# Optimization experiments

Measured on AMD Instinct MI355X. Metric: run time of the kernel, lower is better.

Reference implementation:

```python
import jax, jax.numpy as jnp
import numpy as np

N_NODES = 100000
N_EDGES = 1600000
IN_CH = 128
HEADS = 4
HID = 32
OUT_CH = 128
NEG_SLOPE = 0.2


def setup_inputs() -> dict:
    key = jax.random.key(0)
    ks = jax.random.split(key, 7)
    sc = 1.0 / np.sqrt(IN_CH)
    return {
        "x": jax.random.normal(ks[0], (N_NODES, IN_CH), dtype=jnp.float32),
        "edge_index": jax.random.randint(ks[1], (2, N_EDGES), 0, N_NODES, dtype=jnp.int32),
        "W": jax.random.normal(ks[2], (IN_CH, HEADS * HID), dtype=jnp.float32) * sc,
        "att_src": jax.random.normal(ks[3], (HEADS, HID), dtype=jnp.float32) * sc,
        "att_dst": jax.random.normal(ks[4], (HEADS, HID), dtype=jnp.float32) * sc,
        "lin_w": jax.random.normal(ks[5], (HEADS * HID, OUT_CH), dtype=jnp.float32) * (1.0 / np.sqrt(HEADS * HID)),
        "lin_b": jax.random.normal(ks[6], (OUT_CH,), dtype=jnp.float32) * 0.01,
    }


def reference(x, edge_index, W, att_src, att_dst, lin_w, lin_b):
    N = x.shape[0]
    src, dst = edge_index[0], edge_index[1]
    # node-wise linear transform -> [N, H, C]
    h = (x @ W).reshape(N, HEADS, HID)
    # per-node attention logit components [N, H]
    a_src = jnp.einsum("nhc,hc->nh", h, att_src)
    a_dst = jnp.einsum("nhc,hc->nh", h, att_dst)
    # per-edge logits with LeakyReLU [E, H]
    e = jax.nn.leaky_relu(a_src[src] + a_dst[dst], negative_slope=NEG_SLOPE)
    # segment softmax over destination neighborhoods
    m = jax.ops.segment_max(e, dst, num_segments=N)
    ex = jnp.exp(e - m[dst])
    s = jax.ops.segment_sum(ex, dst, num_segments=N)
    alpha = ex / (s[dst] + 1e-16)
    # weighted scatter-sum of source features [N, H, C] -> concat heads
    msg = h[src] * alpha[:, :, None]
    out = jax.ops.segment_sum(msg, dst, num_segments=N).reshape(N, HEADS * HID)
    # trailing dense + ReLU
    return jax.nn.relu(out @ lin_w + lin_b)
```

## Files before the change

kernel.cpp:

```cpp
#include <hip/hip_runtime.h>
#include <hip/hip_fp16.h>

#define NB   256
#define NBLK 128
#define BSH  9

typedef _Float16 f16;
typedef _Float16 half8 __attribute__((ext_vector_type(8)));
typedef __fp16 pk16x2 __attribute__((ext_vector_type(2)));
typedef float f32x4 __attribute__((ext_vector_type(4)));

__global__ void k_prep(const float* __restrict__ W, const float* __restrict__ LW,
                       f16* __restrict__ Wt, f16* __restrict__ LWt)
{
    int n = blockIdx.x & 127;
    const float* src = (blockIdx.x < 128) ? W : LW;
    f16* dst = (blockIdx.x < 128) ? Wt : LWt;
    int k = threadIdx.x;
    dst[n * 128 + k] = (f16)src[k * 128 + n];
}

__global__ __launch_bounds__(256) void k_gemm_att(
    const float* __restrict__ A, const f16* __restrict__ Wt,
    const float* __restrict__ att_s, const float* __restrict__ att_d,
    f16* __restrict__ Hh, float* __restrict__ as_out, float* __restrict__ ad_out,
    int M)
{
    __shared__ __align__(16) f16 as_lds[64 * 136];
    int t = threadIdx.x;
    int row0 = blockIdx.x * 64;

    {
        int r = t >> 2, kq = (t & 3) * 32;
        const float* ap = A + (size_t)(row0 + r) * 128 + kq;
        bool valid = (row0 + r) < M;
        pk16x2 hb[16];
#pragma unroll
        for (int j = 0; j < 8; ++j) {
            float4 v = valid ? *(const float4*)(ap + j * 4) : make_float4(0.f, 0.f, 0.f, 0.f);
            hb[2 * j]     = __builtin_amdgcn_cvt_pkrtz(v.x, v.y);
            hb[2 * j + 1] = __builtin_amdgcn_cvt_pkrtz(v.z, v.w);
        }
        f16* dst = as_lds + r * 136 + kq;
#pragma unroll
        for (int j = 0; j < 4; ++j) *(float4*)(dst + j * 8) = ((float4*)hb)[j];
    }
    __syncthreads();

    int w = t >> 6, ln = t & 63;
    int rr = (w & 1) * 32;
    int cc = (w >> 1) * 64;
    int q = ln >> 4, m = ln & 15;

    f32x4 acc[2][4];
#pragma unroll
    for (int i = 0; i < 2; ++i)
#pragma unroll
        for (int j = 0; j < 4; ++j) acc[i][j] = (f32x4){0.f, 0.f, 0.f, 0.f};

    const f16* wp = Wt + (size_t)(cc + m) * 128 + q * 8;
#pragma unroll
    for (int ks = 0; ks < 4; ++ks) {
        int k0 = ks * 32 + q * 8;
        half8 a0 = *(const half8*)(as_lds + (rr + m) * 136 + k0);
        half8 a1 = *(const half8*)(as_lds + (rr + 16 + m) * 136 + k0);
        half8 bf[4];
#pragma unroll
        for (int j = 0; j < 4; ++j)
            bf[j] = *(const half8*)(wp + j * 16 * 128 + ks * 32);
#pragma unroll
        for (int j = 0; j < 4; ++j) {
            acc[0][j] = __builtin_amdgcn_mfma_f32_16x16x32_f16(a0, bf[j], acc[0][j], 0, 0, 0);
            acc[1][j] = __builtin_amdgcn_mfma_f32_16x16x32_f16(a1, bf[j], acc[1][j], 0, 0, 0);
        }
    }
    __syncthreads();
#pragma unroll
    for (int i = 0; i < 2; ++i)
#pragma unroll
        for (int j = 0; j < 4; ++j)
#pragma unroll
            for (int g = 0; g < 4; ++g)
                as_lds[(rr + i * 16 + q * 4 + g) * 136 + cc + j * 16 + m] = (f16)acc[i][j][g];
    __syncthreads();
    {
        int r = t >> 2, cq = (t & 3) * 32;
        if (row0 + r < M) {
            float4 o0 = *(const float4*)(as_lds + r * 136 + cq);
            float4 o1 = *(const float4*)(as_lds + r * 136 + cq + 8);
            float4 o2 = *(const float4*)(as_lds + r * 136 + cq + 16);
            float4 o3 = *(const float4*)(as_lds + r * 136 + cq + 24);
            float4* hp = (float4*)(Hh + (size_t)(row0 + r) * 128 + cq);
            hp[0] = o0; hp[1] = o1; hp[2] = o2; hp[3] = o3;
        }
    }
    {
        int rl = w * 16 + m;
        int head = q;
        float ds = 0.f, dd = 0.f;
#pragma unroll
        for (int ch = 0; ch < 4; ++ch) {
            half8 hv = *(const half8*)(as_lds + rl * 136 + head * 32 + ch * 8);
            float4 s0 = *(const float4*)(att_s + head * 32 + ch * 8);
            float4 s1 = *(const float4*)(att_s + head * 32 + ch * 8 + 4);
            float4 d0 = *(const float4*)(att_d + head * 32 + ch * 8);
            float4 d1 = *(const float4*)(att_d + head * 32 + ch * 8 + 4);
            ds += (float)hv[0] * s0.x + (float)hv[1] * s0.y + (float)hv[2] * s0.z + (float)hv[3] * s0.w
                + (float)hv[4] * s1.x + (float)hv[5] * s1.y + (float)hv[6] * s1.z + (float)hv[7] * s1.w;
            dd += (float)hv[0] * d0.x + (float)hv[1] * d0.y + (float)hv[2] * d0.z + (float)hv[3] * d0.w
                + (float)hv[4] * d1.x + (float)hv[5] * d1.y + (float)hv[6] * d1.z + (float)hv[7] * d1.w;
        }
        if (row0 + rl < M) {
            as_out[(row0 + rl) * 4 + head] = ds;
            ad_out[(row0 + rl) * 4 + head] = dd;
        }
    }
}

__global__ __launch_bounds__(256) void k_gemm_bias_relu(
    const f16* __restrict__ Ah, const f16* __restrict__ LWt,
    const float* __restrict__ bias, float* __restrict__ Out, int M)
{
    __shared__ __align__(16) f16 as_lds[64 * 136];
    int t = threadIdx.x;
    int row0 = blockIdx.x * 64;
    {
        int r = t >> 2, kq = (t & 3) * 32;
        f16* dst = as_lds + r * 136 + kq;
        if (row0 + r < M) {
            const float4* ap = (const float4*)(Ah + (size_t)(row0 + r) * 128 + kq);
#pragma unroll
            for (int j = 0; j < 4; ++j) *(float4*)(dst + j * 8) = ap[j];
        } else {
            float4 z = make_float4(0.f, 0.f, 0.f, 0.f);
#pragma unroll
            for (int j = 0; j < 4; ++j) *(float4*)(dst + j * 8) = z;
        }
    }
    __syncthreads();

    int w = t >> 6, ln = t & 63;
    int rr = (w & 1) * 32;
    int cc = (w >> 1) * 64;
    int q = ln >> 4, m = ln & 15;

    f32x4 acc[2][4];
#pragma unroll
    for (int i = 0; i < 2; ++i)
#pragma unroll
        for (int j = 0; j < 4; ++j) acc[i][j] = (f32x4){0.f, 0.f, 0.f, 0.f};

    const f16* wp = LWt + (size_t)(cc + m) * 128 + q * 8;
#pragma unroll
    for (int ks = 0; ks < 4; ++ks) {
        int k0 = ks * 32 + q * 8;
        half8 a0 = *(const half8*)(as_lds + (rr + m) * 136 + k0);
        half8 a1 = *(const half8*)(as_lds + (rr + 16 + m) * 136 + k0);
        half8 bf[4];
#pragma unroll
        for (int j = 0; j < 4; ++j)
            bf[j] = *(const half8*)(wp + j * 16 * 128 + ks * 32);
#pragma unroll
        for (int j = 0; j < 4; ++j) {
            acc[0][j] = __builtin_amdgcn_mfma_f32_16x16x32_f16(a0, bf[j], acc[0][j], 0, 0, 0);
            acc[1][j] = __builtin_amdgcn_mfma_f32_16x16x32_f16(a1, bf[j], acc[1][j], 0, 0, 0);
        }
    }
    float bv[4];
#pragma unroll
    for (int j = 0; j < 4; ++j) bv[j] = bias[cc + j * 16 + m];
#pragma unroll
    for (int i = 0; i < 2; ++i)
#pragma unroll
        for (int g = 0; g < 4; ++g) {
            int row = row0 + rr + i * 16 + q * 4 + g;
            if (row < M) {
#pragma unroll
                for (int j = 0; j < 4; ++j)
                    Out[(size_t)row * 128 + cc + j * 16 + m] = fmaxf(acc[i][j][g] + bv[j], 0.f);
            }
        }
}


__global__ __launch_bounds__(256) void k_ph_hist(
    const int* __restrict__ dst, int* __restrict__ bh, int E, int chunk)
{
    __shared__ int hist[NB];
    int t = threadIdx.x;
    hist[t] = 0;
    __syncthreads();
    int e0 = blockIdx.x * chunk;
    int e1 = min(e0 + chunk, E);
    for (int e = e0 + t; e < e1; e += 256)
        atomicAdd(&hist[dst[e] >> BSH], 1);
    __syncthreads();
    bh[t * NBLK + blockIdx.x] = hist[t];
}

__global__ __launch_bounds__(1024) void k_ph_scan(int* __restrict__ bh)
{
    __shared__ int sd[1024];
    const int per = (NB * NBLK) / 1024;
    int t = threadIdx.x;
    int base = t * per;
    int loc[per];
    int sum = 0;
#pragma unroll
    for (int j = 0; j < per; ++j) { loc[j] = bh[base + j]; sum += loc[j]; }
    sd[t] = sum;
    __syncthreads();
    for (int o = 1; o < 1024; o <<= 1) {
        int x = (t >= o) ? sd[t - o] : 0;
        __syncthreads();
        sd[t] += x;
        __syncthreads();
    }
    int run = sd[t] - sum;
#pragma unroll
    for (int j = 0; j < per; ++j) { bh[base + j] = run; run += loc[j]; }
}

__global__ __launch_bounds__(256) void k_ph_bin(
    const int* __restrict__ ei, const int* __restrict__ bh,
    int* __restrict__ binned, int E, int chunk)
{
    __shared__ int boff[NB];
    int t = threadIdx.x;
    boff[t] = bh[t * NBLK + blockIdx.x];
    __syncthreads();
    int e0 = blockIdx.x * chunk;
    int e1 = min(e0 + chunk, E);
    for (int e = e0 + t; e < e1; e += 256) {
        int s = ei[e];
        int d = ei[E + e];
        int p = atomicAdd(&boff[d >> BSH], 1);
        binned[p] = s | ((d & ((1 << BSH) - 1)) << 17);
    }
}

__global__ __launch_bounds__(256) void k_ph_csr(
    const int* __restrict__ binned, const int* __restrict__ bh,
    int* __restrict__ csr, int* __restrict__ off, int* __restrict__ deg,
    int N, int E)
{
    __shared__ int cnt[512], loff[512], sd[256];
    int b = blockIdx.x;
    int lo = b << BSH;
    if (lo >= N) return;
    int t = threadIdx.x;
    int seg = bh[b * NBLK];
    int segend = (b + 1 < NB) ? bh[(b + 1) * NBLK] : E;
    int len = segend - seg;
    cnt[t] = 0; cnt[t + 256] = 0;
    __syncthreads();
    for (int i = t; i < len; i += 256)
        atomicAdd(&cnt[(unsigned)binned[seg + i] >> 17], 1);
    __syncthreads();
    int a0 = cnt[2 * t], a1 = cnt[2 * t + 1];
    int s = a0 + a1;
    sd[t] = s;
    __syncthreads();
    for (int o = 1; o < 256; o <<= 1) {
        int x = (t >= o) ? sd[t - o] : 0;
        __syncthreads();
        sd[t] += x;
        __syncthreads();
    }
    int ex = sd[t] - s;
    loff[2 * t] = ex;
    loff[2 * t + 1] = ex + a0;
    int n0 = lo + 2 * t;
    if (n0 < N)     { off[n0] = seg + ex;          deg[n0] = a0; }
    if (n0 + 1 < N) { off[n0 + 1] = seg + ex + a0; deg[n0 + 1] = a1; }
    __syncthreads();
    for (int i = t; i < len; i += 256) {
        int v = binned[seg + i];
        int p = atomicAdd(&loff[(unsigned)v >> 17], 1);
        csr[seg + p] = v & 0x1ffff;
    }
}

__global__ __launch_bounds__(256) void k_gather(
    const __half* __restrict__ Hh, const float* __restrict__ as_,
    const float* __restrict__ ad_, const int* __restrict__ off,
    const int* __restrict__ deg, const int* __restrict__ csr,
    __half* __restrict__ P, int N)
{
    __shared__ __align__(16) __half2 wh[16][68];
    __shared__ int srcs[16][16];
    int t = threadIdx.x;
    int wid = t >> 6, lane = t & 63;
    int sub = lane >> 4;
    int li = lane & 15;
    int hh = li >> 2;
    int slot = wid * 4 + sub;
    int n = blockIdx.x * 16 + slot;
    bool nvalid = n < N;
    int dg = nvalid ? deg[n] : 0;
    int base = nvalid ? off[n] : 0;
    float4 adn = nvalid ? *(const float4*)(ad_ + (size_t)n * 4)
                        : make_float4(0.f, 0.f, 0.f, 0.f);

    float s0 = 0.f, s1 = 0.f, s2 = 0.f, s3 = 0.f;
    float acc[8] = {0.f, 0.f, 0.f, 0.f, 0.f, 0.f, 0.f, 0.f};

    for (int c0 = 0; c0 < dg; c0 += 16) {
        int cnt = min(16, dg - c0);
        {
            int idx = c0 + li;
            int se = csr[base + min(idx, dg - 1)];
            float4 as = *(const float4*)(as_ + (size_t)se * 4);
            float e0 = as.x + adn.x, e1 = as.y + adn.y;
            float e2 = as.z + adn.z, e3 = as.w + adn.w;
            e0 = fmaxf(e0, 0.2f * e0); e1 = fmaxf(e1, 0.2f * e1);
            e2 = fmaxf(e2, 0.2f * e2); e3 = fmaxf(e3, 0.2f * e3);
            float x0 = __expf(e0), x1 = __expf(e1);
            float x2 = __expf(e2), x3 = __expf(e3);
            if (idx >= dg) { x0 = x1 = x2 = x3 = 0.f; }
            s0 += x0; s1 += x1; s2 += x2; s3 += x3;
            __half2 w4[4];
            w4[0] = __float2half2_rn(x0);
            w4[1] = __float2half2_rn(x1);
            w4[2] = __float2half2_rn(x2);
            w4[3] = __float2half2_rn(x3);
            *(float4*)&wh[slot][li * 4] = *(float4*)w4;
            srcs[slot][li] = se;
        }
        __asm__ volatile("s_waitcnt lgkmcnt(0)" ::: "memory");
        int quads = (cnt + 3) >> 2;
        __half2 ah[4];
        ah[0] = ah[1] = ah[2] = ah[3] = __float2half2_rn(0.f);
        for (int qq = 0; qq < quads; ++qq) {
#pragma unroll
            for (int u = 0; u < 4; ++u) {
                int i = qq * 4 + u;
                __half2 w2 = wh[slot][i * 4 + hh];
                int se = srcs[slot][i];
                float4 raw = *(const float4*)(Hh + (size_t)se * 128 + li * 8);
                __half2* ph = (__half2*)&raw;
                ah[0] = __hfma2(ph[0], w2, ah[0]);
                ah[1] = __hfma2(ph[1], w2, ah[1]);
                ah[2] = __hfma2(ph[2], w2, ah[2]);
                ah[3] = __hfma2(ph[3], w2, ah[3]);
            }
            if ((qq & 1) == 1) {
#pragma unroll
                for (int k = 0; k < 4; ++k) {
                    float2 f = __half22float2(ah[k]);
                    acc[2 * k] += f.x; acc[2 * k + 1] += f.y;
                    ah[k] = __float2half2_rn(0.f);
                }
            }
        }
#pragma unroll
        for (int k = 0; k < 4; ++k) {
            float2 f = __half22float2(ah[k]);
            acc[2 * k] += f.x; acc[2 * k + 1] += f.y;
        }
        __asm__ volatile("s_waitcnt lgkmcnt(0)" ::: "memory");
    }

#pragma unroll
    for (int o = 1; o < 16; o <<= 1) {
        s0 += __shfl_xor(s0, o);
        s1 += __shfl_xor(s1, o);
        s2 += __shfl_xor(s2, o);
        s3 += __shfl_xor(s3, o);
    }
    float sh = (hh == 0) ? s0 : (hh == 1) ? s1 : (hh == 2) ? s2 : s3;
    float inv = 1.f / (sh + 1e-16f);
    if (nvalid) {
        __half2 o4[4];
#pragma unroll
        for (int k = 0; k < 4; ++k)
            o4[k] = __float22half2_rn(make_float2(acc[2 * k] * inv, acc[2 * k + 1] * inv));
        *(float4*)(P + (size_t)n * 128 + li * 8) = *(float4*)o4;
    }
}


extern "C" void kernel_launch(void* const* d_in, const int* in_sizes, int n_in,
                              void* d_out, int out_size, void* d_ws, size_t ws_size,
                              hipStream_t stream)
{
    const float* x     = (const float*)d_in[0];
    const int*   ei    = (const int*)d_in[1];
    const float* W     = (const float*)d_in[2];
    const float* att_s = (const float*)d_in[3];
    const float* att_d = (const float*)d_in[4];
    const float* lin_w = (const float*)d_in[5];
    const float* lin_b = (const float*)d_in[6];
    float* out = (float*)d_out;
    int N = in_sizes[0] / 128;
    int E = in_sizes[1] / 2;

    char* p = (char*)d_ws;
    auto alloc = [&](size_t bytes) { char* r = p; p += (bytes + 255) & ~(size_t)255; return r; };
    f16*    Hh   = (f16*)alloc((size_t)N * 128 * 2);
    f16*    P    = (f16*)alloc((size_t)N * 128 * 2);
    f16*    Wt   = (f16*)alloc(128 * 128 * 2);
    f16*    LWt  = (f16*)alloc(128 * 128 * 2);
    float*  AS   = (float*)alloc((size_t)N * 4 * 4);
    float*  AD   = (float*)alloc((size_t)N * 4 * 4);
    int*    deg  = (int*)alloc((size_t)N * 4);
    int*    off  = (int*)alloc((size_t)N * 4);
    int*    csr  = (int*)alloc((size_t)E * 4);
    int*    binned = (int*)alloc((size_t)E * 4);
    int*    bh   = (int*)alloc((size_t)NB * NBLK * 4);

    int chunk = (E + NBLK - 1) / NBLK;
    int mb = (N + 63) / 64;
    k_prep<<<256, 128, 0, stream>>>(W, lin_w, Wt, LWt);
    k_gemm_att<<<mb, 256, 0, stream>>>(x, Wt, att_s, att_d, Hh, AS, AD, N);
    k_ph_hist<<<NBLK, 256, 0, stream>>>(ei + E, bh, E, chunk);
    k_ph_scan<<<1, 1024, 0, stream>>>(bh);
    k_ph_bin<<<NBLK, 256, 0, stream>>>(ei, bh, binned, E, chunk);
    k_ph_csr<<<NB, 256, 0, stream>>>(binned, bh, csr, off, deg, N, E);
    k_gather<<<(N + 15) / 16, 256, 0, stream>>>((const __half*)Hh, AS, AD, off, deg, csr, (__half*)P, N);
    k_gemm_bias_relu<<<mb, 256, 0, stream>>>(P, LWt, lin_b, out, N);
}
```

Baseline: 311.4 us.

## Fuse output GEMM into gather and sort nodes by degree for balance

The trailing dense+bias+ReLU GEMM is folded into the gather kernel: each block stages its 16 aggregated rows in LDS and runs MFMA against the output weights, which removes the fp16 intermediate P write and reread and one launch. Nodes are also reordered by degree through a counting sort (histogram, scan, scatter kernels) so that each block processes nodes of similar degree and warps diverge less. The cost is three extra small kernels, including a single-block scan, a tiny 16-row GEMM per block that reloads the weights from global memory, and scattered output row writes.

```diff
diff --git a/kernel.cpp b/kernel.cpp
--- a/kernel.cpp
+++ b/kernel.cpp
@@ -4,6 +4,8 @@
 #define NB   256
 #define NBLK 128
 #define BSH  9
+#define DB   64
+#define DBLK 128
 
 typedef _Float16 f16;
 typedef _Float16 half8 __attribute__((ext_vector_type(8)));
@@ -117,71 +119,6 @@
     }
 }
 
-__global__ __launch_bounds__(256) void k_gemm_bias_relu(
-    const f16* __restrict__ Ah, const f16* __restrict__ LWt,
-    const float* __restrict__ bias, float* __restrict__ Out, int M)
-{
-    __shared__ __align__(16) f16 as_lds[64 * 136];
-    int t = threadIdx.x;
-    int row0 = blockIdx.x * 64;
-    {
-        int r = t >> 2, kq = (t & 3) * 32;
-        f16* dst = as_lds + r * 136 + kq;
-        if (row0 + r < M) {
-            const float4* ap = (const float4*)(Ah + (size_t)(row0 + r) * 128 + kq);
-#pragma unroll
-            for (int j = 0; j < 4; ++j) *(float4*)(dst + j * 8) = ap[j];
-        } else {
-            float4 z = make_float4(0.f, 0.f, 0.f, 0.f);
-#pragma unroll
-            for (int j = 0; j < 4; ++j) *(float4*)(dst + j * 8) = z;
-        }
-    }
-    __syncthreads();
-
-    int w = t >> 6, ln = t & 63;
-    int rr = (w & 1) * 32;
-    int cc = (w >> 1) * 64;
-    int q = ln >> 4, m = ln & 15;
-
-    f32x4 acc[2][4];
-#pragma unroll
-    for (int i = 0; i < 2; ++i)
-#pragma unroll
-        for (int j = 0; j < 4; ++j) acc[i][j] = (f32x4){0.f, 0.f, 0.f, 0.f};
-
-    const f16* wp = LWt + (size_t)(cc + m) * 128 + q * 8;
-#pragma unroll
-    for (int ks = 0; ks < 4; ++ks) {
-        int k0 = ks * 32 + q * 8;
-        half8 a0 = *(const half8*)(as_lds + (rr + m) * 136 + k0);
-        half8 a1 = *(const half8*)(as_lds + (rr + 16 + m) * 136 + k0);
-        half8 bf[4];
-#pragma unroll
-        for (int j = 0; j < 4; ++j)
-            bf[j] = *(const half8*)(wp + j * 16 * 128 + ks * 32);
-#pragma unroll
-        for (int j = 0; j < 4; ++j) {
-            acc[0][j] = __builtin_amdgcn_mfma_f32_16x16x32_f16(a0, bf[j], acc[0][j], 0, 0, 0);
-            acc[1][j] = __builtin_amdgcn_mfma_f32_16x16x32_f16(a1, bf[j], acc[1][j], 0, 0, 0);
-        }
-    }
-    float bv[4];
-#pragma unroll
-    for (int j = 0; j < 4; ++j) bv[j] = bias[cc + j * 16 + m];
-#pragma unroll
-    for (int i = 0; i < 2; ++i)
-#pragma unroll
-        for (int g = 0; g < 4; ++g) {
-            int row = row0 + rr + i * 16 + q * 4 + g;
-            if (row < M) {
-#pragma unroll
-                for (int j = 0; j < 4; ++j)
-                    Out[(size_t)row * 128 + cc + j * 16 + m] = fmaxf(acc[i][j][g] + bv[j], 0.f);
-            }
-        }
-}
-
 
 __global__ __launch_bounds__(256) void k_ph_hist(
     const int* __restrict__ dst, int* __restrict__ bh, int E, int chunk)
@@ -281,22 +218,82 @@
     }
 }
 
-__global__ __launch_bounds__(256) void k_gather(
+__global__ __launch_bounds__(256) void k_dhist(
+    const int* __restrict__ deg, int* __restrict__ dh, int N, int chunk)
+{
+    __shared__ int h[DB];
+    int t = threadIdx.x;
+    if (t < DB) h[t] = 0;
+    __syncthreads();
+    int e0 = blockIdx.x * chunk;
+    int e1 = min(e0 + chunk, N);
+    for (int i = e0 + t; i < e1; i += 256)
+        atomicAdd(&h[min(deg[i], DB - 1)], 1);
+    __syncthreads();
+    if (t < DB) dh[t * DBLK + blockIdx.x] = h[t];
+}
+
+__global__ __launch_bounds__(1024) void k_dscan(int* __restrict__ dh)
+{
+    __shared__ int sd[1024];
+    const int per = (DB * DBLK) / 1024;
+    int t = threadIdx.x;
+    int base = t * per;
+    int loc[per];
+    int sum = 0;
+#pragma unroll
+    for (int j = 0; j < per; ++j) { loc[j] = dh[base + j]; sum += loc[j]; }
+    sd[t] = sum;
+    __syncthreads();
+    for (int o = 1; o < 1024; o <<= 1) {
+        int x = (t >= o) ? sd[t - o] : 0;
+        __syncthreads();
+        sd[t] += x;
+        __syncthreads();
+    }
+    int run = sd[t] - sum;
+#pragma unroll
+    for (int j = 0; j < per; ++j) { dh[base + j] = run; run += loc[j]; }
+}
+
+__global__ __launch_bounds__(256) void k_dscat(
+    const int* __restrict__ deg, const int* __restrict__ dh,
+    int* __restrict__ perm, int N, int chunk)
+{
+    __shared__ int boff[DB];
+    int t = threadIdx.x;
+    if (t < DB) boff[t] = dh[t * DBLK + blockIdx.x];
+    __syncthreads();
+    int e0 = blockIdx.x * chunk;
+    int e1 = min(e0 + chunk, N);
+    for (int i = e0 + t; i < e1; i += 256) {
+        int p = atomicAdd(&boff[min(deg[i], DB - 1)], 1);
+        perm[p] = i;
+    }
+}
+
+__global__ __launch_bounds__(256) void k_gather_fused(
     const __half* __restrict__ Hh, const float* __restrict__ as_,
     const float* __restrict__ ad_, const int* __restrict__ off,
     const int* __restrict__ deg, const int* __restrict__ csr,
-    __half* __restrict__ P, int N)
+    const int* __restrict__ perm, const f16* __restrict__ LWt,
+    const float* __restrict__ bias, float* __restrict__ Out, int N)
 {
     __shared__ __align__(16) __half2 wh[16][68];
     __shared__ int srcs[16][16];
+    __shared__ __align__(16) f16 pt[16][136];
+    __shared__ int pnode[16];
     int t = threadIdx.x;
     int wid = t >> 6, lane = t & 63;
     int sub = lane >> 4;
     int li = lane & 15;
     int hh = li >> 2;
     int slot = wid * 4 + sub;
-    int n = blockIdx.x * 16 + slot;
-    bool nvalid = n < N;
+    int gbase = blockIdx.x * 16;
+    if (t < 16) pnode[t] = (gbase + t < N) ? perm[gbase + t] : -1;
+    __syncthreads();
+    int n = pnode[slot];
+    bool nvalid = n >= 0;
     int dg = nvalid ? deg[n] : 0;
     int base = nvalid ? off[n] : 0;
     float4 adn = nvalid ? *(const float4*)(ad_ + (size_t)n * 4)
@@ -370,12 +367,40 @@
     }
     float sh = (hh == 0) ? s0 : (hh == 1) ? s1 : (hh == 2) ? s2 : s3;
     float inv = 1.f / (sh + 1e-16f);
-    if (nvalid) {
+    {
         __half2 o4[4];
 #pragma unroll
         for (int k = 0; k < 4; ++k)
             o4[k] = __float22half2_rn(make_float2(acc[2 * k] * inv, acc[2 * k + 1] * inv));
-        *(float4*)(P + (size_t)n * 128 + li * 8) = *(float4*)o4;
+        *(float4*)&pt[slot][li * 8] = *(float4*)o4;
+    }
+    __syncthreads();
+
+    {
+        int cc = wid * 32;
+        f32x4 acc2[2];
+        acc2[0] = (f32x4){0.f, 0.f, 0.f, 0.f};
+        acc2[1] = (f32x4){0.f, 0.f, 0.f, 0.f};
+        const f16* wp = LWt + (size_t)(cc + li) * 128 + sub * 8;
+#pragma unroll
+        for (int ks = 0; ks < 4; ++ks) {
+            half8 a0 = *(const half8*)&pt[li][ks * 32 + sub * 8];
+            half8 b0 = *(const half8*)(wp + ks * 32);
+            half8 b1 = *(const half8*)(wp + 16 * 128 + ks * 32);
+            acc2[0] = __builtin_amdgcn_mfma_f32_16x16x32_f16(a0, b0, acc2[0], 0, 0, 0);
+            acc2[1] = __builtin_amdgcn_mfma_f32_16x16x32_f16(a0, b1, acc2[1], 0, 0, 0);
+        }
+        float bv0 = bias[cc + li];
+        float bv1 = bias[cc + 16 + li];
+#pragma unroll
+        for (int g = 0; g < 4; ++g) {
+            int r = sub * 4 + g;
+            int node = pnode[r];
+            if (node >= 0) {
+                Out[(size_t)node * 128 + cc + li]      = fmaxf(acc2[0][g] + bv0, 0.f);
+                Out[(size_t)node * 128 + cc + 16 + li] = fmaxf(acc2[1][g] + bv1, 0.f);
+            }
+        }
     }
 }
 
@@ -398,18 +423,20 @@
     char* p = (char*)d_ws;
     auto alloc = [&](size_t bytes) { char* r = p; p += (bytes + 255) & ~(size_t)255; return r; };
     f16*    Hh   = (f16*)alloc((size_t)N * 128 * 2);
-    f16*    P    = (f16*)alloc((size_t)N * 128 * 2);
     f16*    Wt   = (f16*)alloc(128 * 128 * 2);
     f16*    LWt  = (f16*)alloc(128 * 128 * 2);
     float*  AS   = (float*)alloc((size_t)N * 4 * 4);
     float*  AD   = (float*)alloc((size_t)N * 4 * 4);
     int*    deg  = (int*)alloc((size_t)N * 4);
     int*    off  = (int*)alloc((size_t)N * 4);
+    int*    perm = (int*)alloc((size_t)N * 4);
     int*    csr  = (int*)alloc((size_t)E * 4);
     int*    binned = (int*)alloc((size_t)E * 4);
     int*    bh   = (int*)alloc((size_t)NB * NBLK * 4);
+    int*    dh   = (int*)alloc((size_t)DB * DBLK * 4);
 
     int chunk = (E + NBLK - 1) / NBLK;
+    int nchunk = (N + DBLK - 1) / DBLK;
     int mb = (N + 63) / 64;
     k_prep<<<256, 128, 0, stream>>>(W, lin_w, Wt, LWt);
     k_gemm_att<<<mb, 256, 0, stream>>>(x, Wt, att_s, att_d, Hh, AS, AD, N);
@@ -417,6 +444,9 @@
     k_ph_scan<<<1, 1024, 0, stream>>>(bh);
     k_ph_bin<<<NBLK, 256, 0, stream>>>(ei, bh, binned, E, chunk);
     k_ph_csr<<<NB, 256, 0, stream>>>(binned, bh, csr, off, deg, N, E);
-    k_gather<<<(N + 15) / 16, 256, 0, stream>>>((const __half*)Hh, AS, AD, off, deg, csr, (__half*)P, N);
-    k_gemm_bias_relu<<<mb, 256, 0, stream>>>(P, LWt, lin_b, out, N);
-}
+    k_dhist<<<DBLK, 256, 0, stream>>>(deg, dh, N, nchunk);
+    k_dscan<<<1, 1024, 0, stream>>>(dh);
+    k_dscat<<<DBLK, 256, 0, stream>>>(deg, dh, perm, N, nchunk);
+    k_gather_fused<<<(N + 15) / 16, 256, 0, stream>>>(
+        (const __half*)Hh, AS, AD, off, deg, csr, perm, LWt, lin_b, out, N);
+}
```

Result: no change. 308.5 us (-0.9%).
